# Optimization experiments

Hardware: AMD Instinct MI355X
Metric: run time of the kernel (lower is better)

## Reference

```python
import jax, jax.numpy as jnp
import numpy as np

B = 65536
D = 1280   # input_dim (ESM2-650M pooled feature dim)
H = 512    # hidden_dim
T = 4      # number of affinity types (Kd, Ki, IC50, EC50)


def setup_inputs() -> dict:
    key = jax.random.key(0)
    ks = jax.random.split(key, 6)
    features = jax.random.normal(ks[0], (B, D), dtype=jnp.float32)
    affinity_type_idx = jax.random.randint(ks[1], (B,), 0, T, dtype=jnp.int32)
    # Per-type head parameters (stacked over the T heads).
    s1 = 1.0 / np.sqrt(D)
    s2 = 1.0 / np.sqrt(H)
    W1 = jax.random.uniform(ks[2], (T, D, H), jnp.float32, -s1, s1)
    b1 = jax.random.uniform(ks[3], (T, H), jnp.float32, -s1, s1)
    w2 = jax.random.uniform(ks[4], (T, H), jnp.float32, -s2, s2)  # Linear(H,1) weight, squeezed
    b2 = jax.random.uniform(ks[5], (T,), jnp.float32, -s2, s2)
    return {"features": features, "affinity_type_idx": affinity_type_idx,
            "W1": W1, "b1": b1, "w2": w2, "b2": b2}


def reference(features, affinity_type_idx, W1, b1, w2, b2):
    # Compute every head for every sample (T is tiny), then select the routed one.
    # h: (B, T, H)
    h = jnp.einsum('bd,tdh->bth', features, W1) + b1
    h = jax.nn.gelu(h, approximate=False)  # torch nn.GELU default = exact erf GELU
    # preds_all: (B, T) — each head's Linear(H, 1) output, squeezed
    preds_all = jnp.einsum('bth,th->bt', h, w2) + b2
    # Route: pick each sample's own affinity-type head.
    preds = jnp.take_along_axis(preds_all, affinity_type_idx[:, None].astype(jnp.int32), axis=1)
    return preds[:, 0]  # (B,)
```

## Files before the change

### kernel.cpp

```cpp
#include <hip/hip_runtime.h>
#include <math.h>

#define NB 65536
#define ND 1280
#define NH 512
#define NT 4

typedef float f32x4 __attribute__((ext_vector_type(4)));
typedef float f32x2 __attribute__((ext_vector_type(2)));
typedef short s16x8 __attribute__((ext_vector_type(8)));
typedef unsigned int u32x2 __attribute__((ext_vector_type(2)));
typedef unsigned int u32x4 __attribute__((ext_vector_type(4)));
typedef unsigned long long ull;
typedef unsigned short u16;

static __device__ __forceinline__ unsigned f2bf1(float x) {
    union { float f; unsigned u; } v; v.f = x;
    return (v.u + 0x7fffu + ((v.u >> 16) & 1u)) >> 16;
}
static __device__ __forceinline__ unsigned packbf(float a, float b) {
    return f2bf1(a) | (f2bf1(b) << 16);
}
static __device__ __forceinline__ s16x8 as_s16x8(u32x4 v) {
    union { u32x4 u; s16x8 s; } x; x.u = v; return x.s;
}
static __device__ __forceinline__ int swz(int a) {
    return a ^ (((a >> 7) & 7) << 4);
}
static __device__ __forceinline__ float gelu_exact(float x) {
    return 0.5f * x * (1.0f + erff(x * 0.70710678118654752f));
}
static __device__ __forceinline__ void gload_lds16(const void* g, void* l) {
    __builtin_amdgcn_global_load_lds(
        (const __attribute__((address_space(1))) unsigned int*)g,
        (__attribute__((address_space(3))) unsigned int*)l, 16, 0, 0);
}

#define SCHEDB __builtin_amdgcn_sched_barrier(0)
#define WAITVM(N) do { asm volatile("s_waitcnt vmcnt(" #N ")" ::: "memory"); SCHEDB; } while (0)

__global__ __launch_bounds__(256) void transpose_kernel(const float* __restrict__ W1,
                                                        u16* __restrict__ Wt) {
    __shared__ float tile[64][65];
    int b = blockIdx.x;
    int dt = b % 20; int r = b / 20; int ht = r & 7; int t = r >> 3;
    int d0 = dt * 64, h0 = ht * 64;
    int tid = threadIdx.x;
    const float* src = W1 + ((size_t)t * ND + d0) * NH + h0;
#pragma unroll
    for (int it = 0; it < 16; ++it) {
        int dl = it * 4 + (tid >> 6);
        tile[dl][tid & 63] = src[(size_t)dl * NH + (tid & 63)];
    }
    __syncthreads();
    int hl = tid >> 2, ds = (tid & 3) * 16;
    unsigned pk[8];
#pragma unroll
    for (int j = 0; j < 8; ++j)
        pk[j] = packbf(tile[ds + 2 * j][hl], tile[ds + 2 * j + 1][hl]);
    u16* dst = Wt + ((size_t)(t * NH + h0 + hl)) * ND + d0 + ds;
    *(u32x4*)dst = (u32x4){pk[0], pk[1], pk[2], pk[3]};
    *(u32x4*)(dst + 8) = (u32x4){pk[4], pk[5], pk[6], pk[7]};
}

__global__ __launch_bounds__(256) void count_kernel(const int* __restrict__ idx,
                                                    int* __restrict__ bc) {
    int tid = threadIdx.x;
    int i = blockIdx.x * 256 + tid;
    int t = idx[i];
    int lane = tid & 63, wave = tid >> 6;
    ull b0 = __ballot(t & 1);
    ull b1 = __ballot(t & 2);
    ull mask = ((t & 1) ? b0 : ~b0) & ((t & 2) ? b1 : ~b1);
    int rank = __popcll(mask & ((1ULL << lane) - 1ULL));
    __shared__ int lc[4][4];
    if (tid < 16) ((int*)lc)[tid] = 0;
    __syncthreads();
    if (rank == 0) lc[wave][t] = __popcll(mask);
    __syncthreads();
    if (tid < 4)
        bc[blockIdx.x * 4 + tid] = lc[0][tid] + lc[1][tid] + lc[2][tid] + lc[3][tid];
}

__global__ __launch_bounds__(256) void scan_kernel(const int* __restrict__ bc,
        int* __restrict__ counts, int* __restrict__ base, int* __restrict__ tmap) {
    __shared__ int segtot[64][4];
    __shared__ int segbase[64][4];
    __shared__ int ttot[4];
    int tid = threadIdx.x;
    int t = tid & 3, seg = tid >> 2;
    int s0 = bc[(seg * 4 + 0) * 4 + t];
    int s1 = bc[(seg * 4 + 1) * 4 + t];
    int s2 = bc[(seg * 4 + 2) * 4 + t];
    int s3 = bc[(seg * 4 + 3) * 4 + t];
    segtot[seg][t] = s0 + s1 + s2 + s3;
    __syncthreads();
    if (tid < 4) {
        int run = 0;
        for (int g = 0; g < 64; ++g) { segbase[g][tid] = run; run += segtot[g][tid]; }
        ttot[tid] = run;
        counts[tid] = run;
    }
    __syncthreads();
    if (tid == 0) {
        int s = 0;
        tmap[0] = 0;
        for (int u = 0; u < 4; ++u) { s += (ttot[u] + 127) >> 7; tmap[u + 1] = s; }
    }
    int toff = 0;
    for (int u = 0; u < 4; ++u) toff += (u < t) ? ttot[u] : 0;
    int run = toff + segbase[seg][t];
    base[(seg * 4 + 0) * 4 + t] = run; run += s0;
    base[(seg * 4 + 1) * 4 + t] = run; run += s1;
    base[(seg * 4 + 2) * 4 + t] = run; run += s2;
    base[(seg * 4 + 3) * 4 + t] = run;
}

__global__ __launch_bounds__(256) void scatter_kernel(const int* __restrict__ idx,
        const int* __restrict__ base, int* __restrict__ perm,
        const float* __restrict__ b2, float* __restrict__ out) {
    int tid = threadIdx.x;
    int i = blockIdx.x * 256 + tid;
    int t = idx[i];
    int lane = tid & 63, wave = tid >> 6;
    ull b0 = __ballot(t & 1);
    ull b1 = __ballot(t & 2);
    ull mask = ((t & 1) ? b0 : ~b0) & ((t & 2) ? b1 : ~b1);
    int rank = __popcll(mask & ((1ULL << lane) - 1ULL));
    __shared__ int lc[4][4];
    if (tid < 16) ((int*)lc)[tid] = 0;
    __syncthreads();
    if (rank == 0) lc[wave][t] = __popcll(mask);
    __syncthreads();
    int pre = 0;
#pragma unroll
    for (int w = 0; w < 4; ++w) pre += (w < wave) ? lc[w][t] : 0;
    perm[base[blockIdx.x * 4 + t] + pre + rank] = i;
    out[i] = b2[t];
}

__global__ __launch_bounds__(256, 3) void gemm_glds(
        const float* __restrict__ feat, const u16* __restrict__ Wt,
        const float* __restrict__ b1, const float* __restrict__ w2,
        const int* __restrict__ perm, const int* __restrict__ counts,
        const int* __restrict__ tmap,
        float* __restrict__ partials, float* __restrict__ out, int use_partials) {
    __shared__ char smem[49152];

    int bx = blockIdx.x;
    int r8 = bx & 7, m8 = bx >> 3;
    int ct = m8 & 3, q = m8 >> 2;
    int tau = q * 8 + r8;
    if (tau >= tmap[4]) return;
    int t = 0;
#pragma unroll
    for (int u = 0; u < 3; ++u) t += (tau >= tmap[u + 1]) ? 1 : 0;
    int tile_m = tau - tmap[t];
    int cnt = counts[t];
    int tilebase = tile_m * 128;
    int off_t = 0;
    for (int u = 0; u < t; ++u) off_t += counts[u];

    int tid = threadIdx.x;
    int lane = tid & 63, wave = tid >> 6;
    int wr = wave >> 1, wc = wave & 1;
    int rl = lane & 15, q0 = lane >> 4;
    int hc0 = ct * 128;

    unsigned asrc[4];
    unsigned axor = (unsigned)(((tid & 7) ^ ((tid >> 3) & 7)) * 4);
#pragma unroll
    for (int p = 0; p < 4; ++p) {
        int r = tilebase + p * 32 + (tid >> 3);
        if (r > cnt - 1) r = cnt - 1;
        asrc[p] = (unsigned)perm[off_t + r] * ND + axor;
    }
    unsigned bsrc[2];
    unsigned bxor = (unsigned)(((tid & 3) ^ ((tid >> 3) & 3)) * 8);
#pragma unroll
    for (int p = 0; p < 2; ++p) {
        int col = p * 64 + (tid >> 2);
        bsrc[p] = (unsigned)(t * NH + hc0 + col) * ND + bxor;
    }
    int ldsw = wave * 1024;

    auto STAGE = [&](int kt, int c) {
        char* ab = smem + c * 16384;
        char* bb = smem + 32768 + c * 8192;
#pragma unroll
        for (int p = 0; p < 4; ++p)
            gload_lds16(feat + asrc[p] + kt * 32, ab + p * 4096 + ldsw);
#pragma unroll
        for (int p = 0; p < 2; ++p)
            gload_lds16(Wt + bsrc[p] + kt * 32, bb + p * 4096 + ldsw);
    };

    int ar0 = (wr * 64 + rl) * 128 + (((q0 * 2)     ^ (rl & 7)) << 4);
    int ar1 = (wr * 64 + rl) * 128 + (((q0 * 2 + 1) ^ (rl & 7)) << 4);
    int br0 = (wc * 64 + rl) * 64  + ((q0 ^ ((rl >> 1) & 3)) << 4);

    f32x4 acc[4][4];
#pragma unroll
    for (int a = 0; a < 4; ++a)
#pragma unroll
        for (int b = 0; b < 4; ++b) acc[a][b] = (f32x4){0.f, 0.f, 0.f, 0.f};

    auto COMPUTE = [&](int c) {
        char* ab = smem + c * 16384;
        char* bb = smem + 32768 + c * 8192;
        f32x4 a0[4], a1[4];
        s16x8 bf[4];
#pragma unroll
        for (int f = 0; f < 4; ++f) {
            a0[f] = *(const f32x4*)(ab + f * 2048 + ar0);
            a1[f] = *(const f32x4*)(ab + f * 2048 + ar1);
            bf[f] = *(const s16x8*)(bb + f * 1024 + br0);
        }
        u32x4 abf[4];
#pragma unroll
        for (int f = 0; f < 4; ++f)
            abf[f] = (u32x4){packbf(a0[f][0], a0[f][1]), packbf(a0[f][2], a0[f][3]),
                             packbf(a1[f][0], a1[f][1]), packbf(a1[f][2], a1[f][3])};
#pragma unroll
        for (int fm = 0; fm < 4; ++fm)
#pragma unroll
            for (int fn = 0; fn < 4; ++fn)
                acc[fm][fn] = __builtin_amdgcn_mfma_f32_16x16x32_bf16(
                    as_s16x8(abf[fm]), bf[fn], acc[fm][fn], 0, 0, 0);
    };

    STAGE(0, 0); SCHEDB;
    STAGE(1, 1); SCHEDB;

#pragma unroll 1
    for (int kt = 0; kt < 36; kt += 2) {
        WAITVM(6);
        __builtin_amdgcn_s_barrier();
        COMPUTE(0);
        __builtin_amdgcn_s_barrier();
        STAGE(kt + 2, 0); SCHEDB;
        WAITVM(6);
        __builtin_amdgcn_s_barrier();
        COMPUTE(1);
        __builtin_amdgcn_s_barrier();
        STAGE(kt + 3, 1); SCHEDB;
    }
    WAITVM(6);
    __builtin_amdgcn_s_barrier();
    COMPUTE(0);
    __builtin_amdgcn_s_barrier();
    STAGE(38, 0); SCHEDB;
    WAITVM(6);
    __builtin_amdgcn_s_barrier();
    COMPUTE(1);
    __builtin_amdgcn_s_barrier();
    STAGE(39, 1); SCHEDB;
    WAITVM(6);
    __builtin_amdgcn_s_barrier();
    COMPUTE(0);
    WAITVM(0);
    __builtin_amdgcn_s_barrier();
    COMPUTE(1);

    float part[4][4];
#pragma unroll
    for (int fm = 0; fm < 4; ++fm)
#pragma unroll
        for (int r = 0; r < 4; ++r) part[fm][r] = 0.f;
#pragma unroll
    for (int fn = 0; fn < 4; ++fn) {
        int h = hc0 + wc * 64 + fn * 16 + rl;
        float b1v = b1[t * NH + h];
        float w2v = w2[t * NH + h];
#pragma unroll
        for (int fm = 0; fm < 4; ++fm)
#pragma unroll
            for (int r = 0; r < 4; ++r) {
                float v = acc[fm][fn][r] + b1v;
                part[fm][r] += gelu_exact(v) * w2v;
            }
    }
#pragma unroll
    for (int m = 1; m <= 8; m <<= 1)
#pragma unroll
        for (int fm = 0; fm < 4; ++fm)
#pragma unroll
            for (int r = 0; r < 4; ++r)
                part[fm][r] += __shfl_xor(part[fm][r], m, 64);

    if (rl == 0) {
        int slot = ct * 2 + wc;
#pragma unroll
        for (int fm = 0; fm < 4; ++fm)
#pragma unroll
            for (int r = 0; r < 4; ++r) {
                int row = wr * 64 + fm * 16 + q0 * 4 + r;
                int gr = tilebase + row;
                if (gr < cnt) {
                    int s = perm[off_t + gr];
                    if (use_partials)
                        partials[(size_t)s * 8 + slot] = part[fm][r];
                    else
                        atomicAdd(&out[s], part[fm][r]);
                }
            }
    }
}

__global__ __launch_bounds__(256, 2) void gemm_fallback(
        const float* __restrict__ feat, const float* __restrict__ W1,
        const float* __restrict__ b1, const float* __restrict__ w2,
        const int* __restrict__ perm, const int* __restrict__ counts,
        float* __restrict__ partials, float* __restrict__ out, int use_partials) {
    __shared__ char smem[32768];
    int bx = blockIdx.x;
    int r8 = bx & 7, m8 = bx >> 3;
    int ct = m8 & 3, q = m8 >> 2;
    int g = q * 8 + r8;
    int t = g >> 9, tile_m = g & 511;
    int cnt = counts[t];
    int tilebase = tile_m * 128;
    if (tilebase >= cnt) return;
    int off_t = 0;
    for (int u = 0; u < t; ++u) off_t += counts[u];

    int tid = threadIdx.x;
    int lane = tid & 63, wave = tid >> 6;
    int wr = wave >> 1, wc = wave & 1;
    int hc0 = ct * 128;

    unsigned aoff[8];
#pragma unroll
    for (int i = 0; i < 8; ++i) {
        int r = tilebase + i * 16 + (tid >> 4);
        if (r > cnt - 1) r = cnt - 1;
        int s = perm[off_t + r];
        aoff[i] = (unsigned)s * ND + (tid & 15) * 4;
    }
    f32x4 acc[4][4];
#pragma unroll
    for (int a = 0; a < 4; ++a)
#pragma unroll
        for (int b = 0; b < 4; ++b) acc[a][b] = (f32x4){0.f, 0.f, 0.f, 0.f};
    f32x4 apf[8];
    int cpair = (tid & 63) * 2;
    int kkbase = tid >> 6;
    const float* wbase = W1 + (size_t)t * ND * NH + hc0 + cpair;
    f32x2 bpf[4][4];
    auto LOADA = [&](int k0) {
#pragma unroll
        for (int i = 0; i < 8; ++i)
            apf[i] = *(const f32x4*)(feat + aoff[i] + k0);
    };
    auto LOADB = [&](int k0) {
#pragma unroll
        for (int qq = 0; qq < 4; ++qq) {
            int d = k0 + (kkbase + qq * 4) * 4;
#pragma unroll
            for (int e = 0; e < 4; ++e)
                bpf[qq][e] = *(const f32x2*)(wbase + (size_t)(d + e) * NH);
        }
    };
    auto WRITEA = [&]() {
#pragma unroll
        for (int i = 0; i < 8; ++i) {
            int row = i * 16 + (tid >> 4);
            u32x2 v;
            v.x = packbf(apf[i][0], apf[i][1]);
            v.y = packbf(apf[i][2], apf[i][3]);
            *(u32x2*)(smem + swz(row * 128 + (tid & 15) * 8)) = v;
        }
    };
    auto WRITEB = [&]() {
#pragma unroll
        for (int qq = 0; qq < 4; ++qq) {
            int kk = kkbase + qq * 4;
#pragma unroll
            for (int j = 0; j < 2; ++j) {
                u32x2 v;
                v.x = packbf(bpf[qq][0][j], bpf[qq][1][j]);
                v.y = packbf(bpf[qq][2][j], bpf[qq][3][j]);
                *(u32x2*)(smem + 16384 + swz((cpair + j) * 128 + kk * 8)) = v;
            }
        }
    };
    auto COMPUTE_KS = [&](int ks) {
        int kbyte = ks * 64 + (lane >> 4) * 16;
        s16x8 af[4], bf[4];
#pragma unroll
        for (int f = 0; f < 4; ++f) {
            int rowA = wr * 64 + f * 16 + (lane & 15);
            af[f] = *(const s16x8*)(smem + swz(rowA * 128 + kbyte));
            int colB = wc * 64 + f * 16 + (lane & 15);
            bf[f] = *(const s16x8*)(smem + 16384 + swz(colB * 128 + kbyte));
        }
#pragma unroll
        for (int fm = 0; fm < 4; ++fm)
#pragma unroll
            for (int fn = 0; fn < 4; ++fn)
                acc[fm][fn] = __builtin_amdgcn_mfma_f32_16x16x32_bf16(
                    af[fm], bf[fn], acc[fm][fn], 0, 0, 0);
    };
    LOADA(0); LOADB(0);
    WRITEA(); WRITEB();
    __syncthreads();
#pragma unroll 1
    for (int kt = 0; kt < 20; ++kt) {
        bool nxt = (kt + 1 < 20);
        if (nxt) LOADA((kt + 1) * 64);
        COMPUTE_KS(0);
        if (nxt) LOADB((kt + 1) * 64);
        COMPUTE_KS(1);
        if (nxt) {
            __syncthreads();
            WRITEA(); WRITEB();
            __syncthreads();
        }
    }
    float part[4][4];
#pragma unroll
    for (int fm = 0; fm < 4; ++fm)
#pragma unroll
        for (int r = 0; r < 4; ++r) part[fm][r] = 0.f;
#pragma unroll
    for (int fn = 0; fn < 4; ++fn) {
        int h = hc0 + wc * 64 + fn * 16 + (lane & 15);
        float b1v = b1[t * NH + h];
        float w2v = w2[t * NH + h];
#pragma unroll
        for (int fm = 0; fm < 4; ++fm)
#pragma unroll
            for (int r = 0; r < 4; ++r) {
                float v = acc[fm][fn][r] + b1v;
                part[fm][r] += gelu_exact(v) * w2v;
            }
    }
#pragma unroll
    for (int m = 1; m <= 8; m <<= 1)
#pragma unroll
        for (int fm = 0; fm < 4; ++fm)
#pragma unroll
            for (int r = 0; r < 4; ++r)
                part[fm][r] += __shfl_xor(part[fm][r], m, 64);
    if ((lane & 15) == 0) {
        int slot = ct * 2 + wc;
#pragma unroll
        for (int fm = 0; fm < 4; ++fm)
#pragma unroll
            for (int r = 0; r < 4; ++r) {
                int row = wr * 64 + fm * 16 + (lane >> 4) * 4 + r;
                int gr = tilebase + row;
                if (gr < cnt) {
                    int s = perm[off_t + gr];
                    if (use_partials)
                        partials[(size_t)s * 8 + slot] = part[fm][r];
                    else
                        atomicAdd(&out[s], part[fm][r]);
                }
            }
    }
}

__global__ __launch_bounds__(256) void reduce_kernel(const float* __restrict__ partials,
        const int* __restrict__ idx, const float* __restrict__ b2,
        float* __restrict__ out) {
    int i = blockIdx.x * 256 + threadIdx.x;
    const float* p = partials + (size_t)i * 8;
    float s = b2[idx[i]];
#pragma unroll
    for (int j = 0; j < 8; ++j) s += p[j];
    out[i] = s;
}

extern "C" void kernel_launch(void* const* d_in, const int* in_sizes, int n_in,
                              void* d_out, int out_size, void* d_ws, size_t ws_size,
                              hipStream_t stream) {
    (void)in_sizes; (void)n_in; (void)out_size;
    const float* feat = (const float*)d_in[0];
    const int*   idx  = (const int*)d_in[1];
    const float* W1   = (const float*)d_in[2];
    const float* b1   = (const float*)d_in[3];
    const float* w2   = (const float*)d_in[4];
    const float* b2   = (const float*)d_in[5];
    float* out = (float*)d_out;

    char* ws = (char*)d_ws;
    int* counts  = (int*)ws;
    int* bc      = (int*)(ws + 64);
    int* base    = (int*)(ws + 64 + 4096);
    int* tmap    = (int*)(ws + 64 + 8192);
    int* perm    = (int*)(ws + 128 + 8192);
    float* partials = (float*)(ws + 128 + 8192 + (size_t)NB * 4);
    u16* Wt = (u16*)(ws + 128 + 8192 + (size_t)NB * 4 + (size_t)NB * 32);
    size_t need_part = 128 + 8192 + (size_t)NB * 4 + (size_t)NB * 32;
    size_t need_full = need_part + (size_t)NT * ND * NH * 2;
    int use_partials = (ws_size >= need_part) ? 1 : 0;
    int use_wt = (ws_size >= need_full) ? 1 : 0;

    if (use_wt)
        transpose_kernel<<<NT * 8 * 20, 256, 0, stream>>>(W1, Wt);
    count_kernel<<<NB / 256, 256, 0, stream>>>(idx, bc);
    scan_kernel<<<1, 256, 0, stream>>>(bc, counts, base, tmap);
    scatter_kernel<<<NB / 256, 256, 0, stream>>>(idx, base, perm, b2, out);
    if (use_wt)
        gemm_glds<<<2080, 256, 0, stream>>>(feat, Wt, b1, w2, perm, counts, tmap,
                                            partials, out, use_partials);
    else
        gemm_fallback<<<8192, 256, 0, stream>>>(feat, W1, b1, w2, perm, counts,
                                                partials, out, use_partials);
    if (use_partials)
        reduce_kernel<<<NB / 256, 256, 0, stream>>>(partials, idx, b2, out);
}
```

Measured before the change: 231.7 us.

## Rewrite routed GEMM as 512-thread 256-row tiles with register-staged prefetch pipeline

After: 428.7 us. +85.0%, slower.

```diff
diff --git a/kernel.cpp b/kernel.cpp
--- a/kernel.cpp
+++ b/kernel.cpp
@@ -21,23 +21,16 @@
 static __device__ __forceinline__ unsigned packbf(float a, float b) {
     return f2bf1(a) | (f2bf1(b) << 16);
 }
-static __device__ __forceinline__ s16x8 as_s16x8(u32x4 v) {
-    union { u32x4 u; s16x8 s; } x; x.u = v; return x.s;
-}
 static __device__ __forceinline__ int swz(int a) {
     return a ^ (((a >> 7) & 7) << 4);
 }
 static __device__ __forceinline__ float gelu_exact(float x) {
     return 0.5f * x * (1.0f + erff(x * 0.70710678118654752f));
 }
-static __device__ __forceinline__ void gload_lds16(const void* g, void* l) {
-    __builtin_amdgcn_global_load_lds(
-        (const __attribute__((address_space(1))) unsigned int*)g,
-        (__attribute__((address_space(3))) unsigned int*)l, 16, 0, 0);
-}
 
 #define SCHEDB __builtin_amdgcn_sched_barrier(0)
 #define WAITVM(N) do { asm volatile("s_waitcnt vmcnt(" #N ")" ::: "memory"); SCHEDB; } while (0)
+#define WAITLG do { asm volatile("s_waitcnt lgkmcnt(0)" ::: "memory"); SCHEDB; } while (0)
 
 __global__ __launch_bounds__(256) void transpose_kernel(const float* __restrict__ W1,
                                                         u16* __restrict__ Wt) {
@@ -105,7 +98,7 @@
     if (tid == 0) {
         int s = 0;
         tmap[0] = 0;
-        for (int u = 0; u < 4; ++u) { s += (ttot[u] + 127) >> 7; tmap[u + 1] = s; }
+        for (int u = 0; u < 4; ++u) { s += (ttot[u] + 255) >> 8; tmap[u + 1] = s; }
     }
     int toff = 0;
     for (int u = 0; u < 4; ++u) toff += (u < t) ? ttot[u] : 0;
@@ -139,65 +132,47 @@
     out[i] = b2[t];
 }
 
-__global__ __launch_bounds__(256, 3) void gemm_glds(
+__global__ __launch_bounds__(512, 2) void gemm_8p(
         const float* __restrict__ feat, const u16* __restrict__ Wt,
         const float* __restrict__ b1, const float* __restrict__ w2,
         const int* __restrict__ perm, const int* __restrict__ counts,
         const int* __restrict__ tmap,
         float* __restrict__ partials, float* __restrict__ out, int use_partials) {
-    __shared__ char smem[49152];
+    __shared__ char smem[65536];
 
     int bx = blockIdx.x;
     int r8 = bx & 7, m8 = bx >> 3;
-    int ct = m8 & 3, q = m8 >> 2;
-    int tau = q * 8 + r8;
+    int ct = m8 & 3;
+    int tau = (m8 >> 2) * 8 + r8;
     if (tau >= tmap[4]) return;
     int t = 0;
 #pragma unroll
     for (int u = 0; u < 3; ++u) t += (tau >= tmap[u + 1]) ? 1 : 0;
     int tile_m = tau - tmap[t];
     int cnt = counts[t];
-    int tilebase = tile_m * 128;
+    int tilebase = tile_m * 256;
     int off_t = 0;
     for (int u = 0; u < t; ++u) off_t += counts[u];
 
     int tid = threadIdx.x;
-    int lane = tid & 63, wave = tid >> 6;
-    int wr = wave >> 1, wc = wave & 1;
+    int lane = tid & 63, wid = tid >> 6;
+    int wr = wid >> 1, wc = wid & 1;
     int rl = lane & 15, q0 = lane >> 4;
-    int hc0 = ct * 128;
-
-    unsigned asrc[4];
-    unsigned axor = (unsigned)(((tid & 7) ^ ((tid >> 3) & 7)) * 4);
-#pragma unroll
-    for (int p = 0; p < 4; ++p) {
-        int r = tilebase + p * 32 + (tid >> 3);
-        if (r > cnt - 1) r = cnt - 1;
-        asrc[p] = (unsigned)perm[off_t + r] * ND + axor;
-    }
-    unsigned bsrc[2];
-    unsigned bxor = (unsigned)(((tid & 3) ^ ((tid >> 3) & 3)) * 8);
-#pragma unroll
-    for (int p = 0; p < 2; ++p) {
-        int col = p * 64 + (tid >> 2);
-        bsrc[p] = (unsigned)(t * NH + hc0 + col) * ND + bxor;
-    }
-    int ldsw = wave * 1024;
-
-    auto STAGE = [&](int kt, int c) {
-        char* ab = smem + c * 16384;
-        char* bb = smem + 32768 + c * 8192;
-#pragma unroll
-        for (int p = 0; p < 4; ++p)
-            gload_lds16(feat + asrc[p] + kt * 32, ab + p * 4096 + ldsw);
-#pragma unroll
-        for (int p = 0; p < 2; ++p)
-            gload_lds16(Wt + bsrc[p] + kt * 32, bb + p * 4096 + ldsw);
-    };
-
-    int ar0 = (wr * 64 + rl) * 128 + (((q0 * 2)     ^ (rl & 7)) << 4);
-    int ar1 = (wr * 64 + rl) * 128 + (((q0 * 2 + 1) ^ (rl & 7)) << 4);
-    int br0 = (wc * 64 + rl) * 64  + ((q0 ^ ((rl >> 1) & 3)) << 4);
+    int hc0 = ct * 128 + wc * 64;
+
+    int arow = tid >> 1;
+    int grow = tilebase + arow; if (grow > cnt - 1) grow = cnt - 1;
+    const float* asrc = feat + (size_t)(unsigned)perm[off_t + grow] * ND + (tid & 1) * 32;
+    int akey = (arow & 7) << 4;
+    int awoff[4];
+#pragma unroll
+    for (int c = 0; c < 4; ++c)
+        awoff[c] = arow * 128 + (((tid & 1) * 64 + c * 16) ^ akey);
+
+    int arb0 = (wr * 64 + rl) * 128 + ((q0 * 16) ^ ((rl & 7) << 4));
+    int arb1 = arb0 ^ 64;
+
+    const u16* bbase = Wt + (size_t)(t * NH + hc0 + rl) * ND + q0 * 8;
 
     f32x4 acc[4][4];
 #pragma unroll
@@ -205,103 +180,139 @@
 #pragma unroll
         for (int b = 0; b < 4; ++b) acc[a][b] = (f32x4){0.f, 0.f, 0.f, 0.f};
 
-    auto COMPUTE = [&](int c) {
-        char* ab = smem + c * 16384;
-        char* bb = smem + 32768 + c * 8192;
-        f32x4 a0[4], a1[4];
-        s16x8 bf[4];
-#pragma unroll
-        for (int f = 0; f < 4; ++f) {
-            a0[f] = *(const f32x4*)(ab + f * 2048 + ar0);
-            a1[f] = *(const f32x4*)(ab + f * 2048 + ar1);
-            bf[f] = *(const s16x8*)(bb + f * 1024 + br0);
-        }
-        u32x4 abf[4];
-#pragma unroll
-        for (int f = 0; f < 4; ++f)
-            abf[f] = (u32x4){packbf(a0[f][0], a0[f][1]), packbf(a0[f][2], a0[f][3]),
-                             packbf(a1[f][0], a1[f][1]), packbf(a1[f][2], a1[f][3])};
-#pragma unroll
-        for (int fm = 0; fm < 4; ++fm)
-#pragma unroll
-            for (int fn = 0; fn < 4; ++fn)
-                acc[fm][fn] = __builtin_amdgcn_mfma_f32_16x16x32_bf16(
-                    as_s16x8(abf[fm]), bf[fn], acc[fm][fn], 0, 0, 0);
-    };
-
-    STAGE(0, 0); SCHEDB;
-    STAGE(1, 1); SCHEDB;
+    f32x4 apf[8];
+    s16x8 bE[4][2], bO[4][2];
+
+#define LOADA(KT) do {                                                          \
+    _Pragma("unroll")                                                           \
+    for (int j = 0; j < 8; ++j)                                                 \
+        apf[j] = *(const f32x4*)(asrc + (KT) * 64 + j * 4);                     \
+} while (0)
+
+#define LOADBH(BS, KT, H) do {                                                  \
+    BS[(H)*2+0][0] = *(const s16x8*)(bbase + (size_t)((H)*2+0)*16*ND + (KT)*64);      \
+    BS[(H)*2+0][1] = *(const s16x8*)(bbase + (size_t)((H)*2+0)*16*ND + (KT)*64 + 32); \
+    BS[(H)*2+1][0] = *(const s16x8*)(bbase + (size_t)((H)*2+1)*16*ND + (KT)*64);      \
+    BS[(H)*2+1][1] = *(const s16x8*)(bbase + (size_t)((H)*2+1)*16*ND + (KT)*64 + 32); \
+} while (0)
+
+#define WRITEA(P) do {                                                          \
+    char* ab_ = smem + (P) * 32768;                                             \
+    _Pragma("unroll")                                                           \
+    for (int c = 0; c < 4; ++c) {                                               \
+        u32x4 v_ = (u32x4){packbf(apf[2*c][0],   apf[2*c][1]),                  \
+                           packbf(apf[2*c][2],   apf[2*c][3]),                  \
+                           packbf(apf[2*c+1][0], apf[2*c+1][1]),                \
+                           packbf(apf[2*c+1][2], apf[2*c+1][3])};               \
+        *(u32x4*)(ab_ + awoff[c]) = v_;                                         \
+    }                                                                           \
+} while (0)
+
+#define PHASE(P, QD, BS) do {                                                   \
+    char* ab_ = smem + (P) * 32768;                                             \
+    s16x8 af00 = *(const s16x8*)(ab_ + arb0 + ((QD)*2+0)*2048);                 \
+    s16x8 af01 = *(const s16x8*)(ab_ + arb1 + ((QD)*2+0)*2048);                 \
+    s16x8 af10 = *(const s16x8*)(ab_ + arb0 + ((QD)*2+1)*2048);                 \
+    s16x8 af11 = *(const s16x8*)(ab_ + arb1 + ((QD)*2+1)*2048);                 \
+    __builtin_amdgcn_s_barrier();                                               \
+    WAITLG;                                                                     \
+    __builtin_amdgcn_s_setprio(1);                                              \
+    _Pragma("unroll")                                                           \
+    for (int nf = 0; nf < 4; ++nf) {                                            \
+        acc[(QD)*2+0][nf] = __builtin_amdgcn_mfma_f32_16x16x32_bf16(af00, BS[nf][0], acc[(QD)*2+0][nf], 0,0,0); \
+        acc[(QD)*2+0][nf] = __builtin_amdgcn_mfma_f32_16x16x32_bf16(af01, BS[nf][1], acc[(QD)*2+0][nf], 0,0,0); \
+        acc[(QD)*2+1][nf] = __builtin_amdgcn_mfma_f32_16x16x32_bf16(af10, BS[nf][0], acc[(QD)*2+1][nf], 0,0,0); \
+        acc[(QD)*2+1][nf] = __builtin_amdgcn_mfma_f32_16x16x32_bf16(af11, BS[nf][1], acc[(QD)*2+1][nf], 0,0,0); \
+    }                                                                           \
+    __builtin_amdgcn_s_setprio(0);                                              \
+    __builtin_amdgcn_s_barrier();                                               \
+} while (0)
+
+#define TILE(KT, P, BCUR, BNXT, STAGEB, ENDMODE) do {                           \
+    if (STAGEB) { LOADBH(BNXT, (KT) + 1, 0); }                                  \
+    PHASE(P, 0, BCUR);                                                          \
+    if (STAGEB) { LOADBH(BNXT, (KT) + 1, 1); }                                  \
+    PHASE(P, 1, BCUR);                                                          \
+    if ((ENDMODE) == 0) {                                                       \
+        WAITVM(8);                 \
+        WRITEA((P) ^ 1);                                                        \
+        LOADA((KT) + 2);                                                        \
+        WAITLG;                           \
+        WAITVM(8);                 \
+        __builtin_amdgcn_s_barrier();                                           \
+    } else if ((ENDMODE) == 1) {                                                \
+        WAITVM(8);                                                              \
+        WRITEA((P) ^ 1);                                                        \
+        WAITLG;                                                                 \
+        WAITVM(0);                                  \
+        __builtin_amdgcn_s_barrier();                                           \
+    }                                                                           \
+} while (0)
+
+    LOADA(0);
+    LOADBH(bE, 0, 0);
+    LOADBH(bE, 0, 1);
+    WAITVM(8);
+    WRITEA(0);
+    LOADA(1);
+    WAITLG;
+    WAITVM(8);
+    __builtin_amdgcn_s_barrier();
 
 #pragma unroll 1
-    for (int kt = 0; kt < 36; kt += 2) {
-        WAITVM(6);
-        __builtin_amdgcn_s_barrier();
-        COMPUTE(0);
-        __builtin_amdgcn_s_barrier();
-        STAGE(kt + 2, 0); SCHEDB;
-        WAITVM(6);
-        __builtin_amdgcn_s_barrier();
-        COMPUTE(1);
-        __builtin_amdgcn_s_barrier();
-        STAGE(kt + 3, 1); SCHEDB;
-    }
-    WAITVM(6);
-    __builtin_amdgcn_s_barrier();
-    COMPUTE(0);
-    __builtin_amdgcn_s_barrier();
-    STAGE(38, 0); SCHEDB;
-    WAITVM(6);
-    __builtin_amdgcn_s_barrier();
-    COMPUTE(1);
-    __builtin_amdgcn_s_barrier();
-    STAGE(39, 1); SCHEDB;
-    WAITVM(6);
-    __builtin_amdgcn_s_barrier();
-    COMPUTE(0);
-    WAITVM(0);
-    __builtin_amdgcn_s_barrier();
-    COMPUTE(1);
+    for (int kt = 0; kt < 18; kt += 2) {
+        TILE(kt,     0, bE, bO, 1, 0);
+        TILE(kt + 1, 1, bO, bE, 1, 0);
+    }
+    TILE(18, 0, bE, bO, 1, 1);
+    TILE(19, 1, bO, bE, 0, 2);
+
+#undef TILE
+#undef PHASE
+#undef WRITEA
+#undef LOADBH
+#undef LOADA
 
     float part[4][4];
 #pragma unroll
-    for (int fm = 0; fm < 4; ++fm)
-#pragma unroll
-        for (int r = 0; r < 4; ++r) part[fm][r] = 0.f;
-#pragma unroll
-    for (int fn = 0; fn < 4; ++fn) {
-        int h = hc0 + wc * 64 + fn * 16 + rl;
+    for (int mf = 0; mf < 4; ++mf)
+#pragma unroll
+        for (int r = 0; r < 4; ++r) part[mf][r] = 0.f;
+#pragma unroll
+    for (int nf = 0; nf < 4; ++nf) {
+        int h = hc0 + nf * 16 + rl;
         float b1v = b1[t * NH + h];
         float w2v = w2[t * NH + h];
 #pragma unroll
-        for (int fm = 0; fm < 4; ++fm)
+        for (int mf = 0; mf < 4; ++mf)
 #pragma unroll
             for (int r = 0; r < 4; ++r) {
-                float v = acc[fm][fn][r] + b1v;
-                part[fm][r] += gelu_exact(v) * w2v;
+                float v = acc[mf][nf][r] + b1v;
+                part[mf][r] += gelu_exact(v) * w2v;
             }
     }
 #pragma unroll
     for (int m = 1; m <= 8; m <<= 1)
 #pragma unroll
-        for (int fm = 0; fm < 4; ++fm)
+        for (int mf = 0; mf < 4; ++mf)
 #pragma unroll
             for (int r = 0; r < 4; ++r)
-                part[fm][r] += __shfl_xor(part[fm][r], m, 64);
+                part[mf][r] += __shfl_xor(part[mf][r], m, 64);
 
     if (rl == 0) {
         int slot = ct * 2 + wc;
 #pragma unroll
-        for (int fm = 0; fm < 4; ++fm)
+        for (int mf = 0; mf < 4; ++mf)
 #pragma unroll
             for (int r = 0; r < 4; ++r) {
-                int row = wr * 64 + fm * 16 + q0 * 4 + r;
+                int row = wr * 64 + mf * 16 + q0 * 4 + r;
                 int gr = tilebase + row;
                 if (gr < cnt) {
                     int s = perm[off_t + gr];
                     if (use_partials)
-                        partials[(size_t)s * 8 + slot] = part[fm][r];
+                        partials[(size_t)s * 8 + slot] = part[mf][r];
                     else
-                        atomicAdd(&out[s], part[fm][r]);
+                        atomicAdd(&out[s], part[mf][r]);
                 }
             }
     }
@@ -503,8 +514,8 @@
     scan_kernel<<<1, 256, 0, stream>>>(bc, counts, base, tmap);
     scatter_kernel<<<NB / 256, 256, 0, stream>>>(idx, base, perm, b2, out);
     if (use_wt)
-        gemm_glds<<<2080, 256, 0, stream>>>(feat, Wt, b1, w2, perm, counts, tmap,
-                                            partials, out, use_partials);
+        gemm_8p<<<1056, 512, 0, stream>>>(feat, Wt, b1, w2, perm, counts, tmap,
+                                          partials, out, use_partials);
     else
         gemm_fallback<<<8192, 256, 0, stream>>>(feat, W1, b1, w2, perm, counts,
                                                 partials, out, use_partials);
```
